# Performance work log

Hardware: AMD Instinct MI355X
Metric: run time of the kernel (lower is better)

The kernel has to match this reference:

```python
import jax, jax.numpy as jnp
import numpy as np

B, T, C, H = 8, 2048, 1024, 64  # batch, time(block_size), n_embd, head_size


def setup_inputs() -> dict:
    key = jax.random.key(0)
    k1, k2, k3, k4 = jax.random.split(key, 4)
    x = jax.random.normal(k1, (B, T, C), dtype=jnp.float32)
    # nn.Linear(n_embd, head_size, bias=False): y = x @ W.T with W [H, C];
    # store as [C, H] so projection is x @ W.
    Wq = jax.random.normal(k2, (C, H), dtype=jnp.float32) * 0.02
    Wk = jax.random.normal(k3, (C, H), dtype=jnp.float32) * 0.02
    Wv = jax.random.normal(k4, (C, H), dtype=jnp.float32) * 0.02
    return {"x": x, "Wq": Wq, "Wk": Wk, "Wv": Wv}


def reference(x, Wq, Wk, Wv):
    # x: [B, T, C]
    Bb, Tt, Cc = x.shape
    q = x @ Wq  # [B, T, H]
    k = x @ Wk  # [B, T, H]
    v = x @ Wv  # [B, T, H]
    # scores = Q @ K^T / sqrt(channels)  -- note: code scales by n_embd, not head_size
    scale = jnp.asarray(Cc, x.dtype) ** 0.5
    scores = jnp.einsum('bth,bsh->bts', q, k) / scale  # [B, T, T]
    # causal mask (decoder=True): lower-triangular allowed
    causal = jnp.tril(jnp.ones((Tt, Tt), dtype=bool))
    scores = jnp.where(causal, scores, -jnp.inf)
    attn = jax.nn.softmax(scores, axis=-1)  # [B, T, T]
    # dropout p=0.0 -> identity
    res = attn @ v  # [B, T, H]
    return res, attn
```

## Files before the change

kernel.cpp:

```cpp
#include <hip/hip_runtime.h>
#include <hip/hip_bf16.h>


typedef __attribute__((ext_vector_type(8))) short bf16x8;
typedef __attribute__((ext_vector_type(4))) float f32x4;

#define NB 8
#define NT 2048
#define NC 1024
#define NH 64

#define VM_DRAIN() asm volatile("s_waitcnt vmcnt(0)" ::: "memory")

__device__ __forceinline__ unsigned short f2bf(float f) {
    unsigned int u = __builtin_bit_cast(unsigned int, f);
    u += 0x7fffu + ((u >> 16) & 1u);
    return (unsigned short)(u >> 16);
}

__device__ __forceinline__ bf16x8 cvt8(float4 a, float4 b) {
    union { bf16x8 v; __hip_bfloat162 h[4]; } u;
    u.h[0] = __float22bfloat162_rn(make_float2(a.x, a.y));
    u.h[1] = __float22bfloat162_rn(make_float2(a.z, a.w));
    u.h[2] = __float22bfloat162_rn(make_float2(b.x, b.y));
    u.h[3] = __float22bfloat162_rn(make_float2(b.z, b.w));
    return u.v;
}

__device__ __forceinline__ void async_ld16(const void* g, const void* l) {
    __builtin_amdgcn_global_load_lds(
        (const __attribute__((address_space(1))) unsigned int*)g,
        (__attribute__((address_space(3))) unsigned int*)(unsigned int)(unsigned long long)l,
        16, 0, 0);
}

__global__ __launch_bounds__(256) void wt_kernel(
        const float* __restrict__ Wq,
        const float* __restrict__ Wk,
        const float* __restrict__ Wv,
        unsigned short* __restrict__ Wt) {
    __shared__ float tile[64][65];
    int m  = blockIdx.x >> 4;
    int k0 = (blockIdx.x & 15) * 64;
    const float* W = (m == 0) ? Wq : ((m == 1) ? Wk : Wv);
    int tid = threadIdx.x;
    for (int i = 0; i < 4; ++i) {
        int f = tid + i * 256;
        int r = f >> 4, c4 = (f & 15) * 4;
        float4 v = *(const float4*)&W[(size_t)(k0 + r) * 64 + c4];
        tile[r][c4 + 0] = v.x; tile[r][c4 + 1] = v.y;
        tile[r][c4 + 2] = v.z; tile[r][c4 + 3] = v.w;
    }
    __syncthreads();
    int n  = tid & 63;
    int kq = (tid >> 6) * 16;
    float scale = (m == 0) ? 0.03125f : 1.0f;
    __attribute__((aligned(16))) unsigned short outv[16];
    for (int j = 0; j < 16; ++j)
        outv[j] = f2bf(tile[kq + j][n] * scale);
    unsigned short* dst = &Wt[(size_t)m * (64 * 1024) + (size_t)n * 1024 + k0 + kq];
    *(uint4*)dst       = *(const uint4*)&outv[0];
    *(uint4*)(dst + 8) = *(const uint4*)&outv[8];
}

__global__ __launch_bounds__(256) void qkv_kernel(
        const float* __restrict__ x,
        const unsigned short* __restrict__ Wt,
        unsigned short* __restrict__ qkv,
        unsigned short* __restrict__ v_t) {
    __shared__ char smem[65536];

    int tid  = threadIdx.x;
    int wave = tid >> 6, lane = tid & 63, quad = lane >> 4, l15 = lane & 15;
    int row0 = blockIdx.x * 32;

    f32x4 acc[2][3];
#pragma unroll
    for (int rt = 0; rt < 2; ++rt)
#pragma unroll
        for (int j = 0; j < 3; ++j) acc[rt][j] = (f32x4){0.f, 0.f, 0.f, 0.f};

#pragma unroll
    for (int i = 0; i < 2; ++i) {
        int s = i * 256 + tid;
        int m = s >> 4, p = s & 15;
        int j = (p & 8) | ((p & 7) ^ (m & 7));
        async_ld16(x + (size_t)(row0 + m) * NC + j * 4,
                   smem + i * 4096 + wave * 1024);
    }
#pragma unroll
    for (int i = 0; i < 6; ++i) {
        int s = i * 256 + tid;
        int n = s >> 3, p = s & 7;
        int j = p ^ (n & 7);
        async_ld16(Wt + (size_t)n * NC + j * 8,
                   smem + 8192 + i * 4096 + wave * 1024);
    }

    int cur = 0;
    for (int kb = 0; kb < 16; ++kb) {
        VM_DRAIN();
        __syncthreads();
        if (kb < 15) {
            char* nb = smem + (cur ^ 1) * 32768;
#pragma unroll
            for (int i = 0; i < 2; ++i) {
                int s = i * 256 + tid;
                int m = s >> 4, p = s & 15;
                int j = (p & 8) | ((p & 7) ^ (m & 7));
                async_ld16(x + (size_t)(row0 + m) * NC + (kb + 1) * 64 + j * 4,
                           nb + i * 4096 + wave * 1024);
            }
#pragma unroll
            for (int i = 0; i < 6; ++i) {
                int s = i * 256 + tid;
                int n = s >> 3, p = s & 7;
                int j = p ^ (n & 7);
                async_ld16(Wt + (size_t)n * NC + (kb + 1) * 64 + j * 8,
                           nb + 8192 + i * 4096 + wave * 1024);
            }
        }
        char* Ab = smem + cur * 32768;
        char* Bb = Ab + 8192;
#pragma unroll
        for (int c = 0; c < 2; ++c) {
            bf16x8 af[2];
#pragma unroll
            for (int rt = 0; rt < 2; ++rt) {
                int m  = rt * 16 + l15;
                int j0 = c * 8 + quad * 2;
                int p0 = (j0 & 8) | ((j0 & 7) ^ (m & 7));
                int p1 = (j0 & 8) | (((j0 + 1) & 7) ^ (m & 7));
                float4 a0 = *(const float4*)(Ab + m * 256 + p0 * 16);
                float4 a1 = *(const float4*)(Ab + m * 256 + p1 * 16);
                af[rt] = cvt8(a0, a1);
            }
#pragma unroll
            for (int jj = 0; jj < 3; ++jj) {
                int n = (wave * 3 + jj) * 16 + l15;
                int p = (c * 4 + quad) ^ (n & 7);
                bf16x8 bf = *(const bf16x8*)(Bb + n * 128 + p * 16);
#pragma unroll
                for (int rt = 0; rt < 2; ++rt)
                    acc[rt][jj] = __builtin_amdgcn_mfma_f32_16x16x32_bf16(
                        af[rt], bf, acc[rt][jj], 0, 0, 0);
            }
        }
        cur ^= 1;
    }

    int b = row0 >> 11;
#pragma unroll
    for (int jj = 0; jj < 3; ++jj) {
        int g   = wave * 3 + jj;
        int mat = g >> 2;
        int col = (g & 3) * 16 + l15;
#pragma unroll
        for (int rt = 0; rt < 2; ++rt) {
            int rowb = row0 + rt * 16 + quad * 4;
            if (mat < 2) {
#pragma unroll
                for (int r = 0; r < 4; ++r)
                    qkv[(size_t)mat * (16384 * 64) + (size_t)(rowb + r) * 64 + col] =
                        f2bf(acc[rt][jj][r]);
            } else {
                union { unsigned long long q; unsigned short us[4]; } pk;
#pragma unroll
                for (int r = 0; r < 4; ++r) pk.us[r] = f2bf(acc[rt][jj][r]);
                *(unsigned long long*)&v_t[((size_t)b * 64 + col) * NT + (rowb & 2047)] = pk.q;
            }
        }
    }
}

__global__ __launch_bounds__(256) void fattn_kernel(
        const unsigned short* __restrict__ qg,
        const unsigned short* __restrict__ kg,
        const unsigned short* __restrict__ vtg,
        float* __restrict__ res,
        float* __restrict__ attn) {
    __shared__ unsigned short kt[2 * 64 * 64];
    __shared__ unsigned short vt[2 * 64 * 64];
    __shared__ float ptf[32 * 68];
    __shared__ float rsred[2][32];
    __shared__ float rinv_s[32];
    char* ktb = (char*)kt;
    char* vtb = (char*)vt;

    int gx  = blockIdx.x;
    int b   = blockIdx.y;
    int rsp = gx & 1;
    int j   = gx >> 1;
    int it  = (b & 4) ? (31 - j) : j;
    int tid = threadIdx.x;
    int wave = tid >> 6, lane = tid & 63, quad = lane >> 4, l15 = lane & 15;
    int wr = wave & 1, wc = wave >> 1;
    int tb = it * 64 + rsp * 32;
    size_t brow = (size_t)b * NT;

    bf16x8 qf[2];
    {
        const unsigned short* qp = qg + (brow + tb + wr * 16 + l15) * NH + quad * 8;
        qf[0] = *(const bf16x8*)qp;
        qf[1] = *(const bf16x8*)(qp + 32);
    }
    int trow[4];
#pragma unroll
    for (int r = 0; r < 4; ++r) trow[r] = tb + wr * 16 + quad * 4 + r;

    float rs[4] = {0.f, 0.f, 0.f, 0.f};
    f32x4 oacc[2];
    oacc[0] = (f32x4){0.f, 0.f, 0.f, 0.f};
    oacc[1] = (f32x4){0.f, 0.f, 0.f, 0.f};

#pragma unroll
    for (int i = 0; i < 2; ++i) {
        int s = i * 256 + tid;
        int r = s >> 3, p = s & 7;
        int jj = p ^ (r & 7);
        async_ld16(kg + (brow + r) * NH + jj * 8,
                   ktb + i * 4096 + wave * 1024);
        async_ld16(vtg + ((size_t)b * 64 + r) * NT + jj * 8,
                   vtb + i * 4096 + wave * 1024);
    }

    int cur = 0;
    for (int st = 0; st <= it; ++st) {
        VM_DRAIN();
        __syncthreads();
        if (st + 1 <= it) {
#pragma unroll
            for (int i = 0; i < 2; ++i) {
                int s = i * 256 + tid;
                int r = s >> 3, p = s & 7;
                int jj = p ^ (r & 7);
                async_ld16(kg + (brow + (st + 1) * 64 + r) * NH + jj * 8,
                           ktb + (cur ^ 1) * 8192 + i * 4096 + wave * 1024);
                async_ld16(vtg + ((size_t)b * 64 + r) * NT + (st + 1) * 64 + jj * 8,
                           vtb + (cur ^ 1) * 8192 + i * 4096 + wave * 1024);
            }
        }
        char* kb = ktb + cur * 8192;
        char* vb = vtb + cur * 8192;

        f32x4 sacc[2];
        sacc[0] = (f32x4){0.f, 0.f, 0.f, 0.f};
        sacc[1] = (f32x4){0.f, 0.f, 0.f, 0.f};
#pragma unroll
        for (int c = 0; c < 2; ++c)
#pragma unroll
            for (int ntl = 0; ntl < 2; ++ntl) {
                int n = wc * 32 + ntl * 16 + l15;
                int p = (c * 4 + quad) ^ (n & 7);
                bf16x8 kf = *(const bf16x8*)(kb + n * 128 + p * 16);
                sacc[ntl] = __builtin_amdgcn_mfma_f32_16x16x32_bf16(
                    qf[c], kf, sacc[ntl], 0, 0, 0);
            }

        bool dia = (st == it);
#pragma unroll
        for (int ntl = 0; ntl < 2; ++ntl) {
            int s_g = st * 64 + wc * 32 + ntl * 16 + l15;
#pragma unroll
            for (int r = 0; r < 4; ++r) {
                float e = __expf(sacc[ntl][r]);
                if (dia && s_g > trow[r]) e = 0.f;
                rs[r] += e;
                ptf[(wr * 16 + quad * 4 + r) * 68 + wc * 32 + ntl * 16 + l15] = e;
            }
        }
        __syncthreads();

#pragma unroll
        for (int k = 0; k < 2; ++k) {
            int f = k * 256 + tid;
            int row = f >> 4, c4 = (f & 15) * 4;
            *(float4*)&attn[(brow + tb + row) * NT + st * 64 + c4] =
                *(const float4*)&ptf[row * 68 + c4];
        }
        if (st < it) {
            float4 z4 = {0.f, 0.f, 0.f, 0.f};
#pragma unroll
            for (int k = 0; k < 2; ++k) {
                int f = k * 256 + tid;
                int row = f >> 4, c4 = (f & 15) * 4;
                *(float4*)&attn[(brow + st * 64 + rsp * 32 + row) * NT + it * 64 + c4] = z4;
            }
        }

#pragma unroll
        for (int c = 0; c < 2; ++c) {
            const float* pp = &ptf[(wr * 16 + l15) * 68 + c * 32 + quad * 8];
            float4 a0 = *(const float4*)pp;
            float4 a1 = *(const float4*)(pp + 4);
            bf16x8 pf = cvt8(a0, a1);
#pragma unroll
            for (int ntl = 0; ntl < 2; ++ntl) {
                int n = wc * 32 + ntl * 16 + l15;
                int p = (c * 4 + quad) ^ (n & 7);
                bf16x8 vf = *(const bf16x8*)(vb + n * 128 + p * 16);
                oacc[ntl] = __builtin_amdgcn_mfma_f32_16x16x32_bf16(
                    pf, vf, oacc[ntl], 0, 0, 0);
            }
        }
        cur ^= 1;
    }

#pragma unroll
    for (int r = 0; r < 4; ++r) {
        float v = rs[r];
        v += __shfl_xor(v, 1, 16);
        v += __shfl_xor(v, 2, 16);
        v += __shfl_xor(v, 4, 16);
        v += __shfl_xor(v, 8, 16);
        if (l15 == 0) rsred[wc][wr * 16 + quad * 4 + r] = v;
    }
    __syncthreads();
    if (tid < 32) rinv_s[tid] = 1.0f / (rsred[0][tid] + rsred[1][tid]);
    __syncthreads();

#pragma unroll
    for (int ntl = 0; ntl < 2; ++ntl)
#pragma unroll
        for (int r = 0; r < 4; ++r)
            res[(size_t)(brow + trow[r]) * NH + wc * 32 + ntl * 16 + l15] =
                oacc[ntl][r] * rinv_s[wr * 16 + quad * 4 + r];

    VM_DRAIN();
    for (int st2 = 0; st2 <= it; ++st2) {
#pragma unroll
        for (int k = 0; k < 2; ++k) {
            int f = k * 256 + tid;
            int row = f >> 4, c4 = (f & 15) * 4;
            float* p = &attn[(brow + tb + row) * NT + st2 * 64 + c4];
            float4 v = *(const float4*)p;
            float sc = rinv_s[row];
            v.x *= sc; v.y *= sc; v.z *= sc; v.w *= sc;
            *(float4*)p = v;
        }
    }
}

extern "C" void kernel_launch(void* const* d_in, const int* in_sizes, int n_in,
                              void* d_out, int out_size, void* d_ws, size_t ws_size,
                              hipStream_t stream) {
    const float* x  = (const float*)d_in[0];
    const float* Wq = (const float*)d_in[1];
    const float* Wk = (const float*)d_in[2];
    const float* Wv = (const float*)d_in[3];

    unsigned short* ws  = (unsigned short*)d_ws;
    unsigned short* Wt  = ws;
    unsigned short* qkv = ws + 3 * 64 * 1024;
    unsigned short* v_t = qkv + 2 * 16384 * 64;

    float* res  = (float*)d_out;
    float* attn = res + (size_t)NB * NT * NH;

    hipLaunchKernelGGL(wt_kernel, dim3(48), dim3(256), 0, stream, Wq, Wk, Wv, Wt);
    hipLaunchKernelGGL(qkv_kernel, dim3(512), dim3(256), 0, stream, x, Wt, qkv, v_t);

    const unsigned short* qg = qkv;
    const unsigned short* kg = qkv + 16384 * 64;

    hipLaunchKernelGGL(fattn_kernel, dim3(64, 8), dim3(256), 0, stream,
                       qg, kg, v_t, res, attn);
}
```

Baseline: 235.8 us.

## Compute softmax row sums in a first QK pass, write normalized attention directly

Adds a first pass over the key tiles that computes only the QK^T scores and the exp row sums, so the normalizer is known before the main loop. The second pass recomputes the scores, scales the probabilities by the reciprocal sum, and writes the final attention values and the PV product directly. This removes the read-modify-write pass that rescaled the whole attention matrix in global memory. In exchange, the K loads and QK MFMAs are done twice. Skipping max subtraction is safe here because the scores are small.

```diff
diff --git a/kernel.cpp b/kernel.cpp
--- a/kernel.cpp
+++ b/kernel.cpp
@@ -209,9 +209,73 @@
     for (int r = 0; r < 4; ++r) trow[r] = tb + wr * 16 + quad * 4 + r;
 
     float rs[4] = {0.f, 0.f, 0.f, 0.f};
-    f32x4 oacc[2];
-    oacc[0] = (f32x4){0.f, 0.f, 0.f, 0.f};
-    oacc[1] = (f32x4){0.f, 0.f, 0.f, 0.f};
+
+#pragma unroll
+    for (int i = 0; i < 2; ++i) {
+        int s = i * 256 + tid;
+        int r = s >> 3, p = s & 7;
+        int jj = p ^ (r & 7);
+        async_ld16(kg + (brow + r) * NH + jj * 8,
+                   ktb + i * 4096 + wave * 1024);
+    }
+    int cur = 0;
+    for (int st = 0; st <= it; ++st) {
+        VM_DRAIN();
+        __syncthreads();
+        if (st + 1 <= it) {
+#pragma unroll
+            for (int i = 0; i < 2; ++i) {
+                int s = i * 256 + tid;
+                int r = s >> 3, p = s & 7;
+                int jj = p ^ (r & 7);
+                async_ld16(kg + (brow + (st + 1) * 64 + r) * NH + jj * 8,
+                           ktb + (cur ^ 1) * 8192 + i * 4096 + wave * 1024);
+            }
+        }
+        char* kb = ktb + cur * 8192;
+
+        f32x4 sacc[2];
+        sacc[0] = (f32x4){0.f, 0.f, 0.f, 0.f};
+        sacc[1] = (f32x4){0.f, 0.f, 0.f, 0.f};
+#pragma unroll
+        for (int c = 0; c < 2; ++c)
+#pragma unroll
+            for (int ntl = 0; ntl < 2; ++ntl) {
+                int n = wc * 32 + ntl * 16 + l15;
+                int p = (c * 4 + quad) ^ (n & 7);
+                bf16x8 kf = *(const bf16x8*)(kb + n * 128 + p * 16);
+                sacc[ntl] = __builtin_amdgcn_mfma_f32_16x16x32_bf16(
+                    qf[c], kf, sacc[ntl], 0, 0, 0);
+            }
+        bool dia = (st == it);
+#pragma unroll
+        for (int ntl = 0; ntl < 2; ++ntl) {
+            int s_g = st * 64 + wc * 32 + ntl * 16 + l15;
+#pragma unroll
+            for (int r = 0; r < 4; ++r) {
+                float e = __expf(sacc[ntl][r]);
+                if (dia && s_g > trow[r]) e = 0.f;
+                rs[r] += e;
+            }
+        }
+        cur ^= 1;
+    }
+
+#pragma unroll
+    for (int r = 0; r < 4; ++r) {
+        float v = rs[r];
+        v += __shfl_xor(v, 1, 16);
+        v += __shfl_xor(v, 2, 16);
+        v += __shfl_xor(v, 4, 16);
+        v += __shfl_xor(v, 8, 16);
+        if (l15 == 0) rsred[wc][wr * 16 + quad * 4 + r] = v;
+    }
+    __syncthreads();
+    if (tid < 32) rinv_s[tid] = 1.0f / (rsred[0][tid] + rsred[1][tid]);
+    __syncthreads();
+    float rinv[4];
+#pragma unroll
+    for (int r = 0; r < 4; ++r) rinv[r] = rinv_s[wr * 16 + quad * 4 + r];
 
 #pragma unroll
     for (int i = 0; i < 2; ++i) {
@@ -223,8 +287,11 @@
         async_ld16(vtg + ((size_t)b * 64 + r) * NT + jj * 8,
                    vtb + i * 4096 + wave * 1024);
     }
-
-    int cur = 0;
+    cur = 0;
+    f32x4 oacc[2];
+    oacc[0] = (f32x4){0.f, 0.f, 0.f, 0.f};
+    oacc[1] = (f32x4){0.f, 0.f, 0.f, 0.f};
+
     for (int st = 0; st <= it; ++st) {
         VM_DRAIN();
         __syncthreads();
@@ -263,10 +330,9 @@
             int s_g = st * 64 + wc * 32 + ntl * 16 + l15;
 #pragma unroll
             for (int r = 0; r < 4; ++r) {
-                float e = __expf(sacc[ntl][r]);
-                if (dia && s_g > trow[r]) e = 0.f;
-                rs[r] += e;
-                ptf[(wr * 16 + quad * 4 + r) * 68 + wc * 32 + ntl * 16 + l15] = e;
+                float p = __expf(sacc[ntl][r]) * rinv[r];
+                if (dia && s_g > trow[r]) p = 0.f;
+                ptf[(wr * 16 + quad * 4 + r) * 68 + wc * 32 + ntl * 16 + l15] = p;
             }
         }
         __syncthreads();
@@ -307,38 +373,10 @@
     }
 
 #pragma unroll
-    for (int r = 0; r < 4; ++r) {
-        float v = rs[r];
-        v += __shfl_xor(v, 1, 16);
-        v += __shfl_xor(v, 2, 16);
-        v += __shfl_xor(v, 4, 16);
-        v += __shfl_xor(v, 8, 16);
-        if (l15 == 0) rsred[wc][wr * 16 + quad * 4 + r] = v;
-    }
-    __syncthreads();
-    if (tid < 32) rinv_s[tid] = 1.0f / (rsred[0][tid] + rsred[1][tid]);
-    __syncthreads();
-
-#pragma unroll
     for (int ntl = 0; ntl < 2; ++ntl)
 #pragma unroll
         for (int r = 0; r < 4; ++r)
-            res[(size_t)(brow + trow[r]) * NH + wc * 32 + ntl * 16 + l15] =
-                oacc[ntl][r] * rinv_s[wr * 16 + quad * 4 + r];
-
-    VM_DRAIN();
-    for (int st2 = 0; st2 <= it; ++st2) {
-#pragma unroll
-        for (int k = 0; k < 2; ++k) {
-            int f = k * 256 + tid;
-            int row = f >> 4, c4 = (f & 15) * 4;
-            float* p = &attn[(brow + tb + row) * NT + st2 * 64 + c4];
-            float4 v = *(const float4*)p;
-            float sc = rinv_s[row];
-            v.x *= sc; v.y *= sc; v.z *= sc; v.w *= sc;
-            *(float4*)p = v;
-        }
-    }
+            res[(size_t)(brow + trow[r]) * NH + wc * 32 + ntl * 16 + l15] = oacc[ntl][r];
 }
 
 extern "C" void kernel_launch(void* const* d_in, const int* in_sizes, int n_in,
```

Result: faster. 220.1 us (-6.7%).
